# Optimization experiments

Hardware: AMD Instinct MI355X
Metric: run time of the kernel (lower is better)

The kernel has to match this reference:

```python
import jax, jax.numpy as jnp
import numpy as np

B, S, H, D, K = 262144, 120, 256, 64, 64  # batch, state_dim, vae_hidden_dim, latent_dim, n_codes


def _lin(k, i, o):
    return jax.random.normal(k, (i, o), jnp.float32) / np.sqrt(i).astype(np.float32)


def setup_inputs() -> dict:
    key = jax.random.key(0)
    ks = jax.random.split(key, 9)
    return {
        "inputs": jax.random.normal(ks[0], (B, S), jnp.float32),
        "enc_w1": _lin(ks[1], S, H), "enc_b1": jnp.zeros((H,), jnp.float32),
        "enc_w2": _lin(ks[2], H, H), "enc_b2": jnp.zeros((H,), jnp.float32),
        "enc_w3": _lin(ks[3], H, D), "enc_b3": jnp.zeros((D,), jnp.float32),
        "codebook": jax.random.uniform(ks[4], (K, D), jnp.float32),  # NearestEmbed weight (rand init)
        "fc3_w": _lin(ks[5], D, H), "fc3_b": jnp.zeros((H,), jnp.float32),
        "fc4_w": _lin(ks[6], H, H), "fc4_b": jnp.zeros((H,), jnp.float32),
        "fc5_w": _lin(ks[7], H, S), "fc5_b": jnp.zeros((S,), jnp.float32),
    }


def _nearest(z, codebook):
    # squared L2 distance via |z|^2 - 2 z.C^T + |c|^2; fused GEMM form
    d = ((z * z).sum(-1, keepdims=True)
         - 2.0 * (z @ codebook.T)
         + (codebook * codebook).sum(-1))  # [B, K]
    idx = jnp.argmin(d, axis=-1)  # [B]
    return codebook[idx], idx


def reference(inputs, enc_w1, enc_b1, enc_w2, enc_b2, enc_w3, enc_b3,
              codebook, fc3_w, fc3_b, fc4_w, fc4_b, fc5_w, fc5_b):
    # encode
    h = jax.nn.relu(inputs @ enc_w1 + enc_b1)
    h = jax.nn.relu(h @ enc_w2 + enc_b2)
    z_e = h @ enc_w3 + enc_b3  # [B, D]
    # emb(z_e, weight_sg=True): straight-through to input, codebook detached
    q, argmin = _nearest(z_e, jax.lax.stop_gradient(codebook))
    z_q = z_e + jax.lax.stop_gradient(q - z_e)
    # emb(z_e.detach()): grads flow only to codebook
    emb, _ = _nearest(jax.lax.stop_gradient(z_e), codebook)
    # decode (recon_type=1)
    r = jax.nn.relu(z_q @ fc3_w + fc3_b)
    r = jax.nn.relu(r @ fc4_w + fc4_b)
    s_hat = r @ fc5_w + fc5_b  # [B, S]
    return s_hat, z_e, emb, argmin
```

## Files before the change

### kernel.cpp

```cpp
#include <hip/hip_runtime.h>


#define B_TOTAL 262144
#define THR 0.02f

typedef float  f32x4 __attribute__((ext_vector_type(4)));
typedef short  s16x8 __attribute__((ext_vector_type(8)));

#define ZB ((size_t)B_TOTAL * 120)
#define EB ((size_t)B_TOTAL * 184)
#define AB ((size_t)B_TOTAL * 248)

#define WS_STAB   0
#define WS_CBT    30720
#define WS_CNORM  47104
#define WS_COUNT  47360
#define WS_LIST   47424
#define WS_PKW1   1096064
#define WS_PKW2   1227136
#define WS_PKE3   1489280
#define WS_PKCB   1554816

static __device__ __forceinline__ unsigned short f2bf(float x) {
    unsigned int u = __float_as_uint(x);
    return (unsigned short)((u + 0x7fffu + ((u >> 16) & 1u)) >> 16);
}
static __device__ __forceinline__ void splitbf(float a, unsigned short& h, unsigned short& s) {
    unsigned hb = __float_as_uint(a) & 0xffff0000u;
    h = (unsigned short)(hb >> 16);
    s = f2bf(a - __uint_as_float(hb));
}
static __device__ __forceinline__ void splitbf_t(float a, unsigned short& h, unsigned short& s) {
    unsigned u = __float_as_uint(a);
    h = (unsigned short)(u >> 16);
    float d = a - __uint_as_float(u & 0xffff0000u);
    s = (unsigned short)(__float_as_uint(d) >> 16);
}
static __device__ __forceinline__ float sqnc(float v) {
    float s = v * v;
    asm volatile("" : "+v"(s));
    return s;
}
static __device__ __forceinline__ float np_sumsq64(const float* a) {
    float r8[8];
#pragma unroll
    for (int j = 0; j < 8; ++j) r8[j] = sqnc(a[j]);
#pragma unroll
    for (int i = 8; i < 64; i += 8)
#pragma unroll
        for (int j = 0; j < 8; ++j) r8[j] += sqnc(a[i + j]);
    return ((r8[0] + r8[1]) + (r8[2] + r8[3])) + ((r8[4] + r8[5]) + (r8[6] + r8[7]));
}

static __device__ __forceinline__ int swz(int row, int col) {
    return row * 256 + ((((col >> 3) ^ (row & 7))) << 3) + (col & 7);
}

__global__ __launch_bounds__(256)
void vq_prep(const float* __restrict__ cb,
             const float* __restrict__ dw3, const float* __restrict__ db3,
             const float* __restrict__ dw4, const float* __restrict__ db4,
             const float* __restrict__ dw5, const float* __restrict__ db5,
             float* __restrict__ s_tab, float* __restrict__ cbT, float* __restrict__ cnorm)
{
    __shared__ float c_row[64];
    __shared__ float u1[256];
    __shared__ float u2[256];
    const int k = blockIdx.x;
    const int t = threadIdx.x;

    if (t < 64) c_row[t] = cb[k * 64 + t];
    __syncthreads();
    {
        float s = 0.f;
        for (int f = 0; f < 64; ++f) s = fmaf(c_row[f], dw3[f * 256 + t], s);
        u1[t] = fmaxf(s + db3[t], 0.f);
    }
    if (t < 64) cbT[t * 64 + k] = c_row[t];
    if (t == 0) cnorm[k] = np_sumsq64(&cb[k * 64]);
    __syncthreads();
    {
        float s = 0.f;
        for (int f = 0; f < 256; ++f) s = fmaf(u1[f], dw4[f * 256 + t], s);
        u2[t] = fmaxf(s + db4[t], 0.f);
    }
    __syncthreads();
    if (t < 120) {
        float o = 0.f;
        for (int f = 0; f < 256; ++f) o = fmaf(u2[f], dw5[f * 120 + t], o);
        s_tab[k * 120 + t] = o + db5[t];
    }
}

__global__ __launch_bounds__(512)
void vq_pack(const float* __restrict__ w1, const float* __restrict__ w2,
             const float* __restrict__ ew3, const float* __restrict__ cbT,
             unsigned short* __restrict__ pw1, unsigned short* __restrict__ pw2,
             unsigned short* __restrict__ pe3, unsigned short* __restrict__ pcb,
             int* __restrict__ flag_count)
{
    const int t = threadIdx.x;
    int f = blockIdx.x;
    if (f == 0 && t == 0) *flag_count = 0;

    const float* src; unsigned short* dst;
    int KSN, nt, ks, srcK, ld;
    if (f < 64)       { src = w1;  dst = pw1; KSN = 4; nt = f >> 2;  ks = f & 3; srcK = 120; ld = 256; }
    else if (f < 192) { f -= 64;  src = w2;  dst = pw2; KSN = 8; nt = f >> 3; ks = f & 7; srcK = 256; ld = 256; }
    else if (f < 224) { f -= 192; src = ew3; dst = pe3; KSN = 8; nt = f >> 3; ks = f & 7; srcK = 256; ld = 64; }
    else              { f -= 224; src = cbT; dst = pcb; KSN = 2; nt = f >> 1; ks = f & 1; srcK = 64;  ld = 64; }

    const int lane = t >> 3, j = t & 7;
    const int k = ks * 32 + (lane >> 4) * 8 + j;
    const int n = nt * 16 + (lane & 15);
    float a = (k < srcK) ? src[k * ld + n] : 0.f;
    unsigned short h, l;
    splitbf(a, h, l);
    const int base = (nt * KSN + ks) * 2 * 512;
    dst[base + t] = h;
    dst[base + 512 + t] = l;
}

__global__ __launch_bounds__(512, 4)
void vq_fast(const float* __restrict__ x,
             const float* __restrict__ b1, const float* __restrict__ b2,
             const float* __restrict__ eb3, const float* __restrict__ cb,
             const float* __restrict__ s_tab, const float* __restrict__ cnorm,
             const unsigned short* __restrict__ pw1, const unsigned short* __restrict__ pw2,
             const unsigned short* __restrict__ pe3, const unsigned short* __restrict__ pcb,
             int* __restrict__ flag_count, int* __restrict__ flag_list,
             float* __restrict__ out)
{
    __shared__ __align__(16) unsigned char smem[32768];
    unsigned short* ph = (unsigned short*)smem;
    unsigned short* pl = (unsigned short*)(smem + 16384);
    unsigned short* zh = (unsigned short*)smem;
    unsigned short* zl = (unsigned short*)(smem + 4608);
    float*          dm = (float*)(smem + 9216);
    int*          idxs = (int*)(smem + 17920);

    const int t = threadIdx.x;
    const int w = t >> 6, l = t & 63;
    const int lr = l & 15;
    const int grow0 = blockIdx.x * 32;

    {
        const float* xb = x + (size_t)grow0 * 120;
        unsigned* ph32 = (unsigned*)ph;
        unsigned* pl32 = (unsigned*)pl;
#pragma unroll
        for (int i = 0; i < 4; ++i) {
            int p = t + 512 * i;
            if (p < 1920) {
                int row = p / 60, c2 = p - row * 60;
                float2 v = *(const float2*)&xb[row * 120 + c2 * 2];
                unsigned u0 = __float_as_uint(v.x);
                unsigned u1 = __float_as_uint(v.y);
                unsigned h0u = u0 & 0xffff0000u;
                unsigned h1u = u1 & 0xffff0000u;
                float d0 = v.x - __uint_as_float(h0u);
                float d1 = v.y - __uint_as_float(h1u);
                int o32 = row * 128 + ((((c2 >> 2) ^ (row & 7))) << 2) + (c2 & 3);
                ph32[o32] = (u0 >> 16) | h1u;
                pl32[o32] = (__float_as_uint(d0) >> 16) | (__float_as_uint(d1) & 0xffff0000u);
            }
        }
        if (t < 128) {
            int row = t >> 2, c2 = 60 + (t & 3);
            int o32 = row * 128 + ((((c2 >> 2) ^ (row & 7))) << 2) + (c2 & 3);
            ph32[o32] = 0u;
            pl32[o32] = 0u;
        }
    }
    __syncthreads();

    {
        f32x4 acc[2][2];
#pragma unroll
        for (int a = 0; a < 2; ++a)
#pragma unroll
            for (int b = 0; b < 2; ++b) acc[a][b] = (f32x4)0.f;

#pragma unroll
        for (int ks = 0; ks < 4; ++ks) {
            const int kb = ks * 32 + (l >> 4) * 8;
            s16x8 ah[2], al[2];
#pragma unroll
            for (int rt = 0; rt < 2; ++rt) {
                const int ro = swz(rt * 16 + lr, kb);
                ah[rt] = *(const s16x8*)&ph[ro];
                al[rt] = *(const s16x8*)&pl[ro];
            }
            s16x8 bh[2], bl[2];
#pragma unroll
            for (int ct = 0; ct < 2; ++ct) {
                const unsigned short* pb = pw1 + ((w * 2 + ct) * 4 + ks) * 1024 + l * 8;
                bh[ct] = *(const s16x8*)pb;
                bl[ct] = *(const s16x8*)(pb + 512);
            }
            __builtin_amdgcn_s_setprio(1);
#pragma unroll
            for (int ct = 0; ct < 2; ++ct)
#pragma unroll
                for (int rt = 0; rt < 2; ++rt) {
                    acc[rt][ct] = __builtin_amdgcn_mfma_f32_16x16x32_bf16(ah[rt], bh[ct], acc[rt][ct], 0, 0, 0);
                    acc[rt][ct] = __builtin_amdgcn_mfma_f32_16x16x32_bf16(ah[rt], bl[ct], acc[rt][ct], 0, 0, 0);
                    acc[rt][ct] = __builtin_amdgcn_mfma_f32_16x16x32_bf16(al[rt], bh[ct], acc[rt][ct], 0, 0, 0);
                }
            __builtin_amdgcn_s_setprio(0);
        }
        __syncthreads();
#pragma unroll
        for (int ct = 0; ct < 2; ++ct) {
            const int col = w * 32 + ct * 16 + lr;
            const float bb = b1[col];
#pragma unroll
            for (int rt = 0; rt < 2; ++rt)
#pragma unroll
                for (int r = 0; r < 4; ++r) {
                    float v = fmaxf(acc[rt][ct][r] + bb, 0.f);
                    unsigned short h, s;
                    splitbf_t(v, h, s);
                    const int row = rt * 16 + (l >> 4) * 4 + r;
                    const int o = swz(row, col);
                    ph[o] = h;
                    pl[o] = s;
                }
        }
    }
    __syncthreads();

    {
        f32x4 acc[2][2];
#pragma unroll
        for (int a = 0; a < 2; ++a)
#pragma unroll
            for (int b = 0; b < 2; ++b) acc[a][b] = (f32x4)0.f;

#pragma unroll
        for (int ks = 0; ks < 8; ++ks) {
            const int kb = ks * 32 + (l >> 4) * 8;
            s16x8 ah[2], al[2];
#pragma unroll
            for (int rt = 0; rt < 2; ++rt) {
                const int ro = swz(rt * 16 + lr, kb);
                ah[rt] = *(const s16x8*)&ph[ro];
                al[rt] = *(const s16x8*)&pl[ro];
            }
            s16x8 bh[2], bl[2];
#pragma unroll
            for (int ct = 0; ct < 2; ++ct) {
                const unsigned short* pb = pw2 + ((w * 2 + ct) * 8 + ks) * 1024 + l * 8;
                bh[ct] = *(const s16x8*)pb;
                bl[ct] = *(const s16x8*)(pb + 512);
            }
            __builtin_amdgcn_s_setprio(1);
#pragma unroll
            for (int ct = 0; ct < 2; ++ct)
#pragma unroll
                for (int rt = 0; rt < 2; ++rt) {
                    acc[rt][ct] = __builtin_amdgcn_mfma_f32_16x16x32_bf16(ah[rt], bh[ct], acc[rt][ct], 0, 0, 0);
                    acc[rt][ct] = __builtin_amdgcn_mfma_f32_16x16x32_bf16(ah[rt], bl[ct], acc[rt][ct], 0, 0, 0);
                    acc[rt][ct] = __builtin_amdgcn_mfma_f32_16x16x32_bf16(al[rt], bh[ct], acc[rt][ct], 0, 0, 0);
                }
            __builtin_amdgcn_s_setprio(0);
        }
        __syncthreads();
#pragma unroll
        for (int ct = 0; ct < 2; ++ct) {
            const int col = w * 32 + ct * 16 + lr;
            const float bb = b2[col];
#pragma unroll
            for (int rt = 0; rt < 2; ++rt)
#pragma unroll
                for (int r = 0; r < 4; ++r) {
                    float v = fmaxf(acc[rt][ct][r] + bb, 0.f);
                    unsigned short h, s;
                    splitbf_t(v, h, s);
                    const int row = rt * 16 + (l >> 4) * 4 + r;
                    const int o = swz(row, col);
                    ph[o] = h;
                    pl[o] = s;
                }
        }
    }
    __syncthreads();

    const int rt3 = (w & 1) * 16;
    const int ct3 = w >> 1;
    {
        f32x4 a3 = (f32x4)0.f;

#pragma unroll
        for (int ks = 0; ks < 8; ++ks) {
            const int kb = ks * 32 + (l >> 4) * 8;
            const int ro = swz(rt3 + lr, kb);
            s16x8 ah = *(const s16x8*)&ph[ro];
            s16x8 al = *(const s16x8*)&pl[ro];
            const unsigned short* pb = pe3 + (ct3 * 8 + ks) * 1024 + l * 8;
            s16x8 bh = *(const s16x8*)pb;
            s16x8 bl = *(const s16x8*)(pb + 512);
            __builtin_amdgcn_s_setprio(1);
            a3 = __builtin_amdgcn_mfma_f32_16x16x32_bf16(ah, bh, a3, 0, 0, 0);
            a3 = __builtin_amdgcn_mfma_f32_16x16x32_bf16(ah, bl, a3, 0, 0, 0);
            a3 = __builtin_amdgcn_mfma_f32_16x16x32_bf16(al, bh, a3, 0, 0, 0);
            __builtin_amdgcn_s_setprio(0);
        }
        __syncthreads();
        {
            const int col = ct3 * 16 + lr;
            const float eb = eb3[col];
#pragma unroll
            for (int r = 0; r < 4; ++r) {
                const int row = rt3 + (l >> 4) * 4 + r;
                float z = a3[r] + eb;
                out[ZB + (size_t)(grow0 + row) * 64 + col] = z;
                unsigned short h, s;
                splitbf_t(z, h, s);
                zh[row * 72 + col] = h;
                zl[row * 72 + col] = s;
            }
        }
    }
    __syncthreads();

    {
        f32x4 a4 = (f32x4)0.f;
#pragma unroll
        for (int ks = 0; ks < 2; ++ks) {
            const int kb = ks * 32 + (l >> 4) * 8;
            const int ro = (rt3 + lr) * 72 + kb;
            s16x8 ah = *(const s16x8*)&zh[ro];
            s16x8 al = *(const s16x8*)&zl[ro];
            const unsigned short* pb = pcb + (ct3 * 2 + ks) * 1024 + l * 8;
            s16x8 bh = *(const s16x8*)pb;
            s16x8 bl = *(const s16x8*)(pb + 512);
            __builtin_amdgcn_s_setprio(1);
            a4 = __builtin_amdgcn_mfma_f32_16x16x32_bf16(ah, bh, a4, 0, 0, 0);
            a4 = __builtin_amdgcn_mfma_f32_16x16x32_bf16(ah, bl, a4, 0, 0, 0);
            a4 = __builtin_amdgcn_mfma_f32_16x16x32_bf16(al, bh, a4, 0, 0, 0);
            __builtin_amdgcn_s_setprio(0);
        }
        {
            const int col = ct3 * 16 + lr;
            const float cn = cnorm[col];
#pragma unroll
            for (int r = 0; r < 4; ++r) {
                const int row = rt3 + (l >> 4) * 4 + r;
                dm[row * 68 + col] = cn - 2.f * a4[r];
            }
        }
    }
    __syncthreads();

    if (t < 32) {
        const float* dr = dm + t * 68;
        float best = dr[0], sec = 3.4e38f;
        int bi = 0;
        for (int j = 1; j < 64; ++j) {
            float v = dr[j];
            if (v < best) { sec = best; best = v; bi = j; }
            else if (v < sec) sec = v;
        }
        idxs[t] = bi;
        out[AB + grow0 + t] = (float)bi;
        if (sec - best < THR) {
            int p = atomicAdd(flag_count, 1);
            if (p < B_TOTAL) flag_list[p] = grow0 + t;
        }
    }
    __syncthreads();

#pragma unroll
    for (int i = 0; i < 4; ++i) {
        int p = t + 512 * i;
        int row = p >> 6, c = p & 63;
        out[EB + (size_t)blockIdx.x * 2048 + p] = cb[idxs[row] * 64 + c];
    }
#pragma unroll
    for (int i = 0; i < 8; ++i) {
        int p = t + 512 * i;
        if (p < 3840) {
            int row = p / 120, c = p - row * 120;
            out[(size_t)blockIdx.x * 3840 + p] = s_tab[idxs[row] * 120 + c];
        }
    }
}

__global__ __launch_bounds__(256)
void vq_exact(const float* __restrict__ x,
              const float* __restrict__ w1, const float* __restrict__ b1,
              const float* __restrict__ w2, const float* __restrict__ b2,
              const float* __restrict__ ew3, const float* __restrict__ eb3,
              const float* __restrict__ cb,
              const float* __restrict__ s_tab,
              const float* __restrict__ cbT, const float* __restrict__ cnorm,
              const int* __restrict__ flag_count, const int* __restrict__ flag_list,
              float* __restrict__ out)
{
    __shared__ float act[256 * 18];
    __shared__ float zrm[16 * 68];
    __shared__ float dmr[16 * 68];
    __shared__ float A_lds[16];
    __shared__ int   idxs[16];
    __shared__ int   rl[16];

    const int t = threadIdx.x;
    int count = *flag_count;
    if (count > B_TOTAL) count = B_TOTAL;

    const int tx = t & 31;
    const int ty = t >> 5;
    const int r0 = ty * 2;
    const int c0 = tx * 8;
    const int c0d = tx * 2;

    for (int base = blockIdx.x * 16; base < count; base += 1024 * 16) {
        if (t < 16) {
            int li = base + t;
            rl[t] = flag_list[li < count ? li : count - 1];
        }
        __syncthreads();

        for (int i = 0; i < 8; ++i) {
            int p = t + 256 * i;
            if (p < 1920) {
                int r = p / 120;
                int c = p - r * 120;
                act[c * 18 + r] = x[(size_t)rl[r] * 120 + c];
            }
        }
        __syncthreads();

        {
            float acc[2][8];
#pragma unroll
            for (int i = 0; i < 2; ++i)
#pragma unroll
                for (int c = 0; c < 8; ++c) acc[i][c] = 0.f;
#pragma unroll 2
            for (int k = 0; k < 120; ++k) {
                const float2 av = *(const float2*)&act[k * 18 + r0];
                const float4 wv0 = *(const float4*)&w1[k * 256 + c0];
                const float4 wv1 = *(const float4*)&w1[k * 256 + c0 + 4];
                const float a[2] = {av.x, av.y};
                const float wv[8] = {wv0.x, wv0.y, wv0.z, wv0.w, wv1.x, wv1.y, wv1.z, wv1.w};
#pragma unroll
                for (int i = 0; i < 2; ++i)
#pragma unroll
                    for (int c = 0; c < 8; ++c) acc[i][c] = fmaf(a[i], wv[c], acc[i][c]);
            }
            __syncthreads();
            const float4 bv0 = *(const float4*)&b1[c0];
            const float4 bv1 = *(const float4*)&b1[c0 + 4];
            const float bb[8] = {bv0.x, bv0.y, bv0.z, bv0.w, bv1.x, bv1.y, bv1.z, bv1.w};
#pragma unroll
            for (int c = 0; c < 8; ++c)
#pragma unroll
                for (int i = 0; i < 2; ++i)
                    act[(c0 + c) * 18 + r0 + i] = fmaxf(acc[i][c] + bb[c], 0.f);
        }
        __syncthreads();

        {
            float acc[2][8];
#pragma unroll
            for (int i = 0; i < 2; ++i)
#pragma unroll
                for (int c = 0; c < 8; ++c) acc[i][c] = 0.f;
#pragma unroll 2
            for (int k = 0; k < 256; ++k) {
                const float2 av = *(const float2*)&act[k * 18 + r0];
                const float4 wv0 = *(const float4*)&w2[k * 256 + c0];
                const float4 wv1 = *(const float4*)&w2[k * 256 + c0 + 4];
                const float a[2] = {av.x, av.y};
                const float wv[8] = {wv0.x, wv0.y, wv0.z, wv0.w, wv1.x, wv1.y, wv1.z, wv1.w};
#pragma unroll
                for (int i = 0; i < 2; ++i)
#pragma unroll
                    for (int c = 0; c < 8; ++c) acc[i][c] = fmaf(a[i], wv[c], acc[i][c]);
            }
            __syncthreads();
            const float4 bv0 = *(const float4*)&b2[c0];
            const float4 bv1 = *(const float4*)&b2[c0 + 4];
            const float bb[8] = {bv0.x, bv0.y, bv0.z, bv0.w, bv1.x, bv1.y, bv1.z, bv1.w};
#pragma unroll
            for (int c = 0; c < 8; ++c)
#pragma unroll
                for (int i = 0; i < 2; ++i)
                    act[(c0 + c) * 18 + r0 + i] = fmaxf(acc[i][c] + bb[c], 0.f);
        }
        __syncthreads();

        {
            float acc2[2][2];
#pragma unroll
            for (int i = 0; i < 2; ++i) { acc2[i][0] = 0.f; acc2[i][1] = 0.f; }
#pragma unroll 2
            for (int k = 0; k < 256; ++k) {
                const float2 av = *(const float2*)&act[k * 18 + r0];
                const float2 wv = *(const float2*)&ew3[k * 64 + c0d];
#pragma unroll
                for (int i = 0; i < 2; ++i) {
                    float a = (i == 0) ? av.x : av.y;
                    acc2[i][0] = fmaf(a, wv.x, acc2[i][0]);
                    acc2[i][1] = fmaf(a, wv.y, acc2[i][1]);
                }
            }
            __syncthreads();
            const float2 bv = *(const float2*)&eb3[c0d];
#pragma unroll
            for (int i = 0; i < 2; ++i) {
                float z0 = acc2[i][0] + bv.x;
                float z1 = acc2[i][1] + bv.y;
                act[(c0d + 0) * 18 + r0 + i] = z0;
                act[(c0d + 1) * 18 + r0 + i] = z1;
                zrm[(r0 + i) * 68 + c0d]     = z0;
                zrm[(r0 + i) * 68 + c0d + 1] = z1;
            }
        }
        __syncthreads();

        if (t < 16) A_lds[t] = np_sumsq64(&zrm[t * 68]);
        __syncthreads();

        {
            float acc3[2][2];
#pragma unroll
            for (int i = 0; i < 2; ++i) { acc3[i][0] = 0.f; acc3[i][1] = 0.f; }
#pragma unroll 2
            for (int k = 0; k < 64; ++k) {
                const float2 av = *(const float2*)&act[k * 18 + r0];
                const float2 wv = *(const float2*)&cbT[k * 64 + c0d];
#pragma unroll
                for (int i = 0; i < 2; ++i) {
                    float a = (i == 0) ? av.x : av.y;
                    acc3[i][0] = fmaf(a, wv.x, acc3[i][0]);
                    acc3[i][1] = fmaf(a, wv.y, acc3[i][1]);
                }
            }
            const float cn0 = cnorm[c0d], cn1 = cnorm[c0d + 1];
#pragma unroll
            for (int i = 0; i < 2; ++i) {
                float g0 = 2.0f * acc3[i][0];  asm volatile("" : "+v"(g0));
                float g1 = 2.0f * acc3[i][1];  asm volatile("" : "+v"(g1));
                const float Ar = A_lds[r0 + i];
                dmr[(r0 + i) * 68 + c0d]     = (Ar - g0) + cn0;
                dmr[(r0 + i) * 68 + c0d + 1] = (Ar - g1) + cn1;
            }
        }
        __syncthreads();

        if (t < 16) {
            const float* dr = &dmr[t * 68];
            float best = dr[0];
            int bi = 0;
            for (int c = 1; c < 64; ++c) {
                float v = dr[c];
                if (v < best) { best = v; bi = c; }
            }
            idxs[t] = bi;
            out[AB + rl[t]] = (float)bi;
        }
        __syncthreads();

        {
            const int r = t >> 4, q = t & 15;
            *(float4*)(out + ZB + (size_t)rl[r] * 64 + q * 4) = *(const float4*)&zrm[r * 68 + q * 4];
        }
        {
            const int r = t >> 4, q = t & 15;
            *(float4*)(out + EB + (size_t)rl[r] * 64 + q * 4) = *(const float4*)(cb + idxs[r] * 64 + q * 4);
        }
        for (int i = 0; i < 8; ++i) {
            int p = t + 256 * i;
            if (p < 1920) {
                int r = p / 120;
                int c = p - r * 120;
                out[(size_t)rl[r] * 120 + c] = s_tab[idxs[r] * 120 + c];
            }
        }
        __syncthreads();
    }
}

extern "C" void kernel_launch(void* const* d_in, const int* in_sizes, int n_in,
                              void* d_out, int out_size, void* d_ws, size_t ws_size,
                              hipStream_t stream)
{
    const float* x   = (const float*)d_in[0];
    const float* w1  = (const float*)d_in[1];
    const float* b1  = (const float*)d_in[2];
    const float* w2  = (const float*)d_in[3];
    const float* b2  = (const float*)d_in[4];
    const float* ew3 = (const float*)d_in[5];
    const float* eb3 = (const float*)d_in[6];
    const float* cb  = (const float*)d_in[7];
    const float* dw3 = (const float*)d_in[8];
    const float* db3 = (const float*)d_in[9];
    const float* dw4 = (const float*)d_in[10];
    const float* db4 = (const float*)d_in[11];
    const float* dw5 = (const float*)d_in[12];
    const float* db5 = (const float*)d_in[13];

    float* out = (float*)d_out;
    char* ws = (char*)d_ws;
    float* s_tab = (float*)(ws + WS_STAB);
    float* cbT   = (float*)(ws + WS_CBT);
    float* cnorm = (float*)(ws + WS_CNORM);
    int*   fcnt  = (int*)(ws + WS_COUNT);
    int*   flist = (int*)(ws + WS_LIST);
    unsigned short* pw1 = (unsigned short*)(ws + WS_PKW1);
    unsigned short* pw2 = (unsigned short*)(ws + WS_PKW2);
    unsigned short* pe3 = (unsigned short*)(ws + WS_PKE3);
    unsigned short* pcb = (unsigned short*)(ws + WS_PKCB);

    vq_prep<<<64, 256, 0, stream>>>(cb, dw3, db3, dw4, db4, dw5, db5,
                                    s_tab, cbT, cnorm);
    vq_pack<<<232, 512, 0, stream>>>(w1, w2, ew3, cbT, pw1, pw2, pe3, pcb, fcnt);
    vq_fast<<<B_TOTAL / 32, 512, 0, stream>>>(x, b1, b2, eb3, cb, s_tab, cnorm,
                                              pw1, pw2, pe3, pcb, fcnt, flist, out);
    vq_exact<<<1024, 256, 0, stream>>>(x, w1, b1, w2, b2, ew3, eb3, cb,
                                       s_tab, cbT, cnorm, fcnt, flist, out);
}
```

Before: 444.2 us.

## Fold codebook distance GEMM into encoder layer 3 via precomputed W3·C^T

Precomputes W3·C^T in the pack kernel, and folds the bias term into the codebook norm as |c|^2 - 2 b3·c. The z·C^T distance GEMM is then computed alongside z_e directly from the layer-2 activations in one K=256 pass. This removes a shared-memory round trip, a sync and the separate K=64 GEMM for the distances. It also re-tiles the first two GEMMs so each wave owns 16 rows by 64 columns instead of 32 by 32, reusing A fragments across more B tiles. The fused product doubles the K depth of the distance MFMAs and changes the rounding of distances, which the exact fallback kernel is relied on to correct.

```diff
diff --git a/kernel.cpp b/kernel.cpp
--- a/kernel.cpp
+++ b/kernel.cpp
@@ -19,7 +19,8 @@
 #define WS_PKW1   1096064
 #define WS_PKW2   1227136
 #define WS_PKE3   1489280
-#define WS_PKCB   1554816
+#define WS_PKW4   1554816
+#define WS_CN2    1620352
 
 static __device__ __forceinline__ unsigned short f2bf(float x) {
     unsigned int u = __float_as_uint(x);
@@ -94,26 +95,47 @@
 
 __global__ __launch_bounds__(512)
 void vq_pack(const float* __restrict__ w1, const float* __restrict__ w2,
-             const float* __restrict__ ew3, const float* __restrict__ cbT,
+             const float* __restrict__ ew3, const float* __restrict__ cb,
+             const float* __restrict__ eb3,
              unsigned short* __restrict__ pw1, unsigned short* __restrict__ pw2,
-             unsigned short* __restrict__ pe3, unsigned short* __restrict__ pcb,
-             int* __restrict__ flag_count)
+             unsigned short* __restrict__ pe3, unsigned short* __restrict__ pw4,
+             float* __restrict__ cn2, int* __restrict__ flag_count)
 {
     const int t = threadIdx.x;
     int f = blockIdx.x;
     if (f == 0 && t == 0) *flag_count = 0;
 
-    const float* src; unsigned short* dst;
-    int KSN, nt, ks, srcK, ld;
-    if (f < 64)       { src = w1;  dst = pw1; KSN = 4; nt = f >> 2;  ks = f & 3; srcK = 120; ld = 256; }
-    else if (f < 192) { f -= 64;  src = w2;  dst = pw2; KSN = 8; nt = f >> 3; ks = f & 7; srcK = 256; ld = 256; }
-    else if (f < 224) { f -= 192; src = ew3; dst = pe3; KSN = 8; nt = f >> 3; ks = f & 7; srcK = 256; ld = 64; }
-    else              { f -= 224; src = cbT; dst = pcb; KSN = 2; nt = f >> 1; ks = f & 1; srcK = 64;  ld = 64; }
-
     const int lane = t >> 3, j = t & 7;
-    const int k = ks * 32 + (lane >> 4) * 8 + j;
-    const int n = nt * 16 + (lane & 15);
-    float a = (k < srcK) ? src[k * ld + n] : 0.f;
+    float a;
+    unsigned short* dst;
+    int nt, ks, KSN;
+
+    if (f < 224) {
+        const float* src; int srcK, ld;
+        if (f < 64)       { src = w1;  dst = pw1; KSN = 4; nt = f >> 2;  ks = f & 3; srcK = 120; ld = 256; }
+        else if (f < 192) { f -= 64;  src = w2;  dst = pw2; KSN = 8; nt = f >> 3; ks = f & 7; srcK = 256; ld = 256; }
+        else              { f -= 192; src = ew3; dst = pe3; KSN = 8; nt = f >> 3; ks = f & 7; srcK = 256; ld = 64; }
+        const int k = ks * 32 + (lane >> 4) * 8 + j;
+        const int n = nt * 16 + (lane & 15);
+        a = (k < srcK) ? src[k * ld + n] : 0.f;
+    } else {
+        int g = f - 224;
+        dst = pw4; KSN = 8; nt = g >> 3; ks = g & 7;
+        const int k = ks * 32 + (lane >> 4) * 8 + j;
+        const int n = nt * 16 + (lane & 15);
+        float s = 0.f;
+        const float* er = ew3 + k * 64;
+        const float* cr = cb + n * 64;
+        for (int d = 0; d < 64; ++d) s = fmaf(er[d], cr[d], s);
+        a = s;
+        if (g == 0 && t < 64) {
+            float ss = 0.f, e2 = 0.f;
+            const float* c = cb + t * 64;
+            for (int d = 0; d < 64; ++d) { ss = fmaf(c[d], c[d], ss); e2 = fmaf(eb3[d], c[d], e2); }
+            cn2[t] = ss - 2.f * e2;
+        }
+    }
+
     unsigned short h, l;
     splitbf(a, h, l);
     const int base = (nt * KSN + ks) * 2 * 512;
@@ -125,19 +147,17 @@
 void vq_fast(const float* __restrict__ x,
              const float* __restrict__ b1, const float* __restrict__ b2,
              const float* __restrict__ eb3, const float* __restrict__ cb,
-             const float* __restrict__ s_tab, const float* __restrict__ cnorm,
+             const float* __restrict__ s_tab, const float* __restrict__ cn2,
              const unsigned short* __restrict__ pw1, const unsigned short* __restrict__ pw2,
-             const unsigned short* __restrict__ pe3, const unsigned short* __restrict__ pcb,
+             const unsigned short* __restrict__ pe3, const unsigned short* __restrict__ pw4,
              int* __restrict__ flag_count, int* __restrict__ flag_list,
              float* __restrict__ out)
 {
     __shared__ __align__(16) unsigned char smem[32768];
     unsigned short* ph = (unsigned short*)smem;
     unsigned short* pl = (unsigned short*)(smem + 16384);
-    unsigned short* zh = (unsigned short*)smem;
-    unsigned short* zl = (unsigned short*)(smem + 4608);
-    float*          dm = (float*)(smem + 9216);
-    int*          idxs = (int*)(smem + 17920);
+    float*          dm = (float*)smem;
+    int*          idxs = (int*)(smem + 8704);
 
     const int t = threadIdx.x;
     const int w = t >> 6, l = t & 63;
@@ -174,181 +194,144 @@
     }
     __syncthreads();
 
+    const int wrow = w & 1, wcol = w >> 1;
+    const int rA = wrow * 16 + lr;
+
     {
-        f32x4 acc[2][2];
-#pragma unroll
-        for (int a = 0; a < 2; ++a)
-#pragma unroll
-            for (int b = 0; b < 2; ++b) acc[a][b] = (f32x4)0.f;
+        f32x4 acc[4];
+#pragma unroll
+        for (int b = 0; b < 4; ++b) acc[b] = (f32x4)0.f;
 
 #pragma unroll
         for (int ks = 0; ks < 4; ++ks) {
             const int kb = ks * 32 + (l >> 4) * 8;
-            s16x8 ah[2], al[2];
-#pragma unroll
-            for (int rt = 0; rt < 2; ++rt) {
-                const int ro = swz(rt * 16 + lr, kb);
-                ah[rt] = *(const s16x8*)&ph[ro];
-                al[rt] = *(const s16x8*)&pl[ro];
-            }
-            s16x8 bh[2], bl[2];
-#pragma unroll
-            for (int ct = 0; ct < 2; ++ct) {
-                const unsigned short* pb = pw1 + ((w * 2 + ct) * 4 + ks) * 1024 + l * 8;
-                bh[ct] = *(const s16x8*)pb;
-                bl[ct] = *(const s16x8*)(pb + 512);
-            }
-            __builtin_amdgcn_s_setprio(1);
-#pragma unroll
-            for (int ct = 0; ct < 2; ++ct)
-#pragma unroll
-                for (int rt = 0; rt < 2; ++rt) {
-                    acc[rt][ct] = __builtin_amdgcn_mfma_f32_16x16x32_bf16(ah[rt], bh[ct], acc[rt][ct], 0, 0, 0);
-                    acc[rt][ct] = __builtin_amdgcn_mfma_f32_16x16x32_bf16(ah[rt], bl[ct], acc[rt][ct], 0, 0, 0);
-                    acc[rt][ct] = __builtin_amdgcn_mfma_f32_16x16x32_bf16(al[rt], bh[ct], acc[rt][ct], 0, 0, 0);
+            const int ro = swz(rA, kb);
+            s16x8 ah = *(const s16x8*)&ph[ro];
+            s16x8 al = *(const s16x8*)&pl[ro];
+#pragma unroll
+            for (int cp = 0; cp < 2; ++cp) {
+                s16x8 bh[2], bl[2];
+#pragma unroll
+                for (int j = 0; j < 2; ++j) {
+                    const unsigned short* pb = pw1 + ((wcol * 4 + cp * 2 + j) * 4 + ks) * 1024 + l * 8;
+                    bh[j] = *(const s16x8*)pb;
+                    bl[j] = *(const s16x8*)(pb + 512);
                 }
-            __builtin_amdgcn_s_setprio(0);
-        }
-        __syncthreads();
-#pragma unroll
-        for (int ct = 0; ct < 2; ++ct) {
-            const int col = w * 32 + ct * 16 + lr;
+                __builtin_amdgcn_s_setprio(1);
+#pragma unroll
+                for (int j = 0; j < 2; ++j) {
+                    const int ct = cp * 2 + j;
+                    acc[ct] = __builtin_amdgcn_mfma_f32_16x16x32_bf16(ah, bh[j], acc[ct], 0, 0, 0);
+                    acc[ct] = __builtin_amdgcn_mfma_f32_16x16x32_bf16(ah, bl[j], acc[ct], 0, 0, 0);
+                    acc[ct] = __builtin_amdgcn_mfma_f32_16x16x32_bf16(al, bh[j], acc[ct], 0, 0, 0);
+                }
+                __builtin_amdgcn_s_setprio(0);
+            }
+        }
+        __syncthreads();
+#pragma unroll
+        for (int ct = 0; ct < 4; ++ct) {
+            const int col = wcol * 64 + ct * 16 + lr;
             const float bb = b1[col];
 #pragma unroll
-            for (int rt = 0; rt < 2; ++rt)
-#pragma unroll
-                for (int r = 0; r < 4; ++r) {
-                    float v = fmaxf(acc[rt][ct][r] + bb, 0.f);
-                    unsigned short h, s;
-                    splitbf_t(v, h, s);
-                    const int row = rt * 16 + (l >> 4) * 4 + r;
-                    const int o = swz(row, col);
-                    ph[o] = h;
-                    pl[o] = s;
-                }
+            for (int r = 0; r < 4; ++r) {
+                float v = fmaxf(acc[ct][r] + bb, 0.f);
+                unsigned short h, s;
+                splitbf_t(v, h, s);
+                const int row = wrow * 16 + (l >> 4) * 4 + r;
+                const int o = swz(row, col);
+                ph[o] = h;
+                pl[o] = s;
+            }
         }
     }
     __syncthreads();
 
     {
-        f32x4 acc[2][2];
-#pragma unroll
-        for (int a = 0; a < 2; ++a)
-#pragma unroll
-            for (int b = 0; b < 2; ++b) acc[a][b] = (f32x4)0.f;
+        f32x4 acc[4];
+#pragma unroll
+        for (int b = 0; b < 4; ++b) acc[b] = (f32x4)0.f;
 
 #pragma unroll
         for (int ks = 0; ks < 8; ++ks) {
             const int kb = ks * 32 + (l >> 4) * 8;
-            s16x8 ah[2], al[2];
-#pragma unroll
-            for (int rt = 0; rt < 2; ++rt) {
-                const int ro = swz(rt * 16 + lr, kb);
-                ah[rt] = *(const s16x8*)&ph[ro];
-                al[rt] = *(const s16x8*)&pl[ro];
-            }
-            s16x8 bh[2], bl[2];
-#pragma unroll
-            for (int ct = 0; ct < 2; ++ct) {
-                const unsigned short* pb = pw2 + ((w * 2 + ct) * 8 + ks) * 1024 + l * 8;
-                bh[ct] = *(const s16x8*)pb;
-                bl[ct] = *(const s16x8*)(pb + 512);
-            }
-            __builtin_amdgcn_s_setprio(1);
-#pragma unroll
-            for (int ct = 0; ct < 2; ++ct)
-#pragma unroll
-                for (int rt = 0; rt < 2; ++rt) {
-                    acc[rt][ct] = __builtin_amdgcn_mfma_f32_16x16x32_bf16(ah[rt], bh[ct], acc[rt][ct], 0, 0, 0);
-                    acc[rt][ct] = __builtin_amdgcn_mfma_f32_16x16x32_bf16(ah[rt], bl[ct], acc[rt][ct], 0, 0, 0);
-                    acc[rt][ct] = __builtin_amdgcn_mfma_f32_16x16x32_bf16(al[rt], bh[ct], acc[rt][ct], 0, 0, 0);
+            const int ro = swz(rA, kb);
+            s16x8 ah = *(const s16x8*)&ph[ro];
+            s16x8 al = *(const s16x8*)&pl[ro];
+#pragma unroll
+            for (int cp = 0; cp < 2; ++cp) {
+                s16x8 bh[2], bl[2];
+#pragma unroll
+                for (int j = 0; j < 2; ++j) {
+                    const unsigned short* pb = pw2 + ((wcol * 4 + cp * 2 + j) * 8 + ks) * 1024 + l * 8;
+                    bh[j] = *(const s16x8*)pb;
+                    bl[j] = *(const s16x8*)(pb + 512);
                 }
-            __builtin_amdgcn_s_setprio(0);
-        }
-        __syncthreads();
-#pragma unroll
-        for (int ct = 0; ct < 2; ++ct) {
-            const int col = w * 32 + ct * 16 + lr;
+                __builtin_amdgcn_s_setprio(1);
+#pragma unroll
+                for (int j = 0; j < 2; ++j) {
+                    const int ct = cp * 2 + j;
+                    acc[ct] = __builtin_amdgcn_mfma_f32_16x16x32_bf16(ah, bh[j], acc[ct], 0, 0, 0);
+                    acc[ct] = __builtin_amdgcn_mfma_f32_16x16x32_bf16(ah, bl[j], acc[ct], 0, 0, 0);
+                    acc[ct] = __builtin_amdgcn_mfma_f32_16x16x32_bf16(al, bh[j], acc[ct], 0, 0, 0);
+                }
+                __builtin_amdgcn_s_setprio(0);
+            }
+        }
+        __syncthreads();
+#pragma unroll
+        for (int ct = 0; ct < 4; ++ct) {
+            const int col = wcol * 64 + ct * 16 + lr;
             const float bb = b2[col];
 #pragma unroll
-            for (int rt = 0; rt < 2; ++rt)
-#pragma unroll
-                for (int r = 0; r < 4; ++r) {
-                    float v = fmaxf(acc[rt][ct][r] + bb, 0.f);
-                    unsigned short h, s;
-                    splitbf_t(v, h, s);
-                    const int row = rt * 16 + (l >> 4) * 4 + r;
-                    const int o = swz(row, col);
-                    ph[o] = h;
-                    pl[o] = s;
-                }
-        }
-    }
-    __syncthreads();
-
-    const int rt3 = (w & 1) * 16;
-    const int ct3 = w >> 1;
+            for (int r = 0; r < 4; ++r) {
+                float v = fmaxf(acc[ct][r] + bb, 0.f);
+                unsigned short h, s;
+                splitbf_t(v, h, s);
+                const int row = wrow * 16 + (l >> 4) * 4 + r;
+                const int o = swz(row, col);
+                ph[o] = h;
+                pl[o] = s;
+            }
+        }
+    }
+    __syncthreads();
+
     {
         f32x4 a3 = (f32x4)0.f;
+        f32x4 a4 = (f32x4)0.f;
 
 #pragma unroll
         for (int ks = 0; ks < 8; ++ks) {
             const int kb = ks * 32 + (l >> 4) * 8;
-            const int ro = swz(rt3 + lr, kb);
+            const int ro = swz(rA, kb);
             s16x8 ah = *(const s16x8*)&ph[ro];
             s16x8 al = *(const s16x8*)&pl[ro];
-            const unsigned short* pb = pe3 + (ct3 * 8 + ks) * 1024 + l * 8;
-            s16x8 bh = *(const s16x8*)pb;
-            s16x8 bl = *(const s16x8*)(pb + 512);
+            const unsigned short* pb3 = pe3 + (wcol * 8 + ks) * 1024 + l * 8;
+            const unsigned short* pb4 = pw4 + (wcol * 8 + ks) * 1024 + l * 8;
+            s16x8 bh3 = *(const s16x8*)pb3;
+            s16x8 bl3 = *(const s16x8*)(pb3 + 512);
+            s16x8 bh4 = *(const s16x8*)pb4;
+            s16x8 bl4 = *(const s16x8*)(pb4 + 512);
             __builtin_amdgcn_s_setprio(1);
-            a3 = __builtin_amdgcn_mfma_f32_16x16x32_bf16(ah, bh, a3, 0, 0, 0);
-            a3 = __builtin_amdgcn_mfma_f32_16x16x32_bf16(ah, bl, a3, 0, 0, 0);
-            a3 = __builtin_amdgcn_mfma_f32_16x16x32_bf16(al, bh, a3, 0, 0, 0);
+            a3 = __builtin_amdgcn_mfma_f32_16x16x32_bf16(ah, bh3, a3, 0, 0, 0);
+            a3 = __builtin_amdgcn_mfma_f32_16x16x32_bf16(ah, bl3, a3, 0, 0, 0);
+            a3 = __builtin_amdgcn_mfma_f32_16x16x32_bf16(al, bh3, a3, 0, 0, 0);
+            a4 = __builtin_amdgcn_mfma_f32_16x16x32_bf16(ah, bh4, a4, 0, 0, 0);
+            a4 = __builtin_amdgcn_mfma_f32_16x16x32_bf16(ah, bl4, a4, 0, 0, 0);
+            a4 = __builtin_amdgcn_mfma_f32_16x16x32_bf16(al, bh4, a4, 0, 0, 0);
             __builtin_amdgcn_s_setprio(0);
         }
         __syncthreads();
-        {
-            const int col = ct3 * 16 + lr;
-            const float eb = eb3[col];
-#pragma unroll
-            for (int r = 0; r < 4; ++r) {
-                const int row = rt3 + (l >> 4) * 4 + r;
-                float z = a3[r] + eb;
-                out[ZB + (size_t)(grow0 + row) * 64 + col] = z;
-                unsigned short h, s;
-                splitbf_t(z, h, s);
-                zh[row * 72 + col] = h;
-                zl[row * 72 + col] = s;
-            }
-        }
-    }
-    __syncthreads();
-
-    {
-        f32x4 a4 = (f32x4)0.f;
-#pragma unroll
-        for (int ks = 0; ks < 2; ++ks) {
-            const int kb = ks * 32 + (l >> 4) * 8;
-            const int ro = (rt3 + lr) * 72 + kb;
-            s16x8 ah = *(const s16x8*)&zh[ro];
-            s16x8 al = *(const s16x8*)&zl[ro];
-            const unsigned short* pb = pcb + (ct3 * 2 + ks) * 1024 + l * 8;
-            s16x8 bh = *(const s16x8*)pb;
-            s16x8 bl = *(const s16x8*)(pb + 512);
-            __builtin_amdgcn_s_setprio(1);
-            a4 = __builtin_amdgcn_mfma_f32_16x16x32_bf16(ah, bh, a4, 0, 0, 0);
-            a4 = __builtin_amdgcn_mfma_f32_16x16x32_bf16(ah, bl, a4, 0, 0, 0);
-            a4 = __builtin_amdgcn_mfma_f32_16x16x32_bf16(al, bh, a4, 0, 0, 0);
-            __builtin_amdgcn_s_setprio(0);
-        }
-        {
-            const int col = ct3 * 16 + lr;
-            const float cn = cnorm[col];
-#pragma unroll
-            for (int r = 0; r < 4; ++r) {
-                const int row = rt3 + (l >> 4) * 4 + r;
-                dm[row * 68 + col] = cn - 2.f * a4[r];
-            }
+
+        const int col = wcol * 16 + lr;
+        const float eb = eb3[col];
+        const float cn = cn2[col];
+#pragma unroll
+        for (int r = 0; r < 4; ++r) {
+            const int row = wrow * 16 + (l >> 4) * 4 + r;
+            out[ZB + (size_t)(grow0 + row) * 64 + col] = a3[r] + eb;
+            dm[row * 68 + col] = cn - 2.f * a4[r];
         }
     }
     __syncthreads();
@@ -613,13 +596,15 @@
     unsigned short* pw1 = (unsigned short*)(ws + WS_PKW1);
     unsigned short* pw2 = (unsigned short*)(ws + WS_PKW2);
     unsigned short* pe3 = (unsigned short*)(ws + WS_PKE3);
-    unsigned short* pcb = (unsigned short*)(ws + WS_PKCB);
+    unsigned short* pw4 = (unsigned short*)(ws + WS_PKW4);
+    float* cn2 = (float*)(ws + WS_CN2);
 
     vq_prep<<<64, 256, 0, stream>>>(cb, dw3, db3, dw4, db4, dw5, db5,
                                     s_tab, cbT, cnorm);
-    vq_pack<<<232, 512, 0, stream>>>(w1, w2, ew3, cbT, pw1, pw2, pe3, pcb, fcnt);
-    vq_fast<<<B_TOTAL / 32, 512, 0, stream>>>(x, b1, b2, eb3, cb, s_tab, cnorm,
-                                              pw1, pw2, pe3, pcb, fcnt, flist, out);
+    vq_pack<<<256, 512, 0, stream>>>(w1, w2, ew3, cb, eb3,
+                                     pw1, pw2, pe3, pw4, cn2, fcnt);
+    vq_fast<<<B_TOTAL / 32, 512, 0, stream>>>(x, b1, b2, eb3, cb, s_tab, cn2,
+                                              pw1, pw2, pe3, pw4, fcnt, flist, out);
     vq_exact<<<1024, 256, 0, stream>>>(x, w1, b1, w2, b2, ew3, eb3, cb,
                                        s_tab, cbT, cnorm, fcnt, flist, out);
 }
```

Result: slower. 539.3 us (+21.4%).
